# Performance work log

Measured on AMD Instinct MI355X. Metric: run time of the kernel, lower is better.

Reference implementation:

```python
import jax, jax.numpy as jnp
import numpy as np
jax.config.update("jax_enable_x64", True)

T_OLD = 60000
T_NEW = 60000
NV = 30000
MAX_STEPS = 300
FB_CHUNK = 500  # T_OLD must be divisible by this

FACE_OPP = np.array([[1, 2, 3], [0, 2, 3], [0, 1, 3], [0, 1, 2]])
EDGES = [(0, 1), (0, 2), (0, 3), (1, 2), (1, 3), (2, 3)]


def setup_inputs() -> dict:
    key = jax.random.key(0)
    k1, k2, k3, k4, k5 = jax.random.split(key, 5)
    # distinct vertices per tet (sorted base + strictly increasing offsets)
    off = jnp.arange(4, dtype=jnp.int64)
    new_indices = jnp.sort(jax.random.randint(k1, (T_NEW, 4), 0, NV - 4, dtype=jnp.int64), axis=1) + off
    old_indices = jnp.sort(jax.random.randint(k2, (T_OLD, 4), 0, NV - 4, dtype=jnp.int64), axis=1) + off
    return {
        "new_indices": new_indices,
        "old_indices": old_indices,
        "old_cc": jax.random.normal(k3, (T_OLD, 3), dtype=jnp.float32),
        "new_cc": jax.random.normal(k4, (T_NEW, 3), dtype=jnp.float32),
        "vertex_positions": jax.random.uniform(k5, (NV, 3), dtype=jnp.float32),
    }


def _min_edge_length(verts, indices):
    p = verts[indices]  # (T,4,3)
    el = jnp.stack([jnp.linalg.norm(p[:, a] - p[:, b], axis=-1) for a, b in EDGES])
    return el.min(axis=0)


def _forward(new_indices, old_indices, old_cc, new_cc, vertex_positions):
    T_new = new_indices.shape[0]
    T_old = old_indices.shape[0]
    Vn = vertex_positions.shape[0]

    # --- 1. unchanged-tet detection via sorted-vertex int64 keys ---
    key4 = lambda s: ((s[:, 0] * Vn + s[:, 1]) * Vn + s[:, 2]) * Vn + s[:, 3]
    ok = key4(jnp.sort(old_indices, axis=1))
    nk = key4(jnp.sort(new_indices, axis=1))
    order = jnp.argsort(ok)
    sk = ok[order]
    pos = jnp.searchsorted(sk, nk, side='right') - 1
    posc = jnp.clip(pos, 0, T_old - 1)
    matched = jnp.where((pos >= 0) & (sk[posc] == nk), order[posc], -1)
    is_matched = matched >= 0
    matched_safe = jnp.maximum(matched, 0)

    # --- 2. face adjacency of old mesh (sorted face keys, adjacent-equal pairing) ---
    fi = jnp.sort(old_indices[:, FACE_OPP], axis=2)          # (T_old,4,3)
    fk = (fi[..., 0] * Vn + fi[..., 1]) * Vn + fi[..., 2]    # (T_old,4)
    all_keys = fk.T.reshape(-1)                              # f-major like the numpy concat
    all_tets = jnp.tile(jnp.arange(T_old), 4)
    all_locals = jnp.repeat(jnp.arange(4), T_old)
    o2 = jnp.argsort(all_keys)
    sk2, st, sl = all_keys[o2], all_tets[o2], all_locals[o2]
    same = sk2[:-1] == sk2[1:]
    neighbors = jnp.full((T_old, 4), -1, dtype=jnp.int64)
    neighbors = neighbors.at[jnp.where(same, st[:-1], T_old), sl[:-1]].set(st[1:], mode='drop')
    neighbors = neighbors.at[jnp.where(same, st[1:], T_old), sl[1:]].set(st[:-1], mode='drop')

    # --- 3. per-old-tet inverse edge matrix; degenerate tets get no neighbors ---
    verts = jax.lax.stop_gradient(vertex_positions).astype(jnp.float32)
    p = verts[old_indices]                                   # (T_old,4,3)
    v0 = p[:, 0]
    Tm = jnp.stack([p[:, 1] - v0, p[:, 2] - v0, p[:, 3] - v0], axis=-1)
    degen = jnp.abs(jnp.linalg.det(Tm)) < 1e-10
    Tinv = jnp.linalg.inv(jnp.where(degen[:, None, None], jnp.eye(3, dtype=Tm.dtype), Tm))
    neighbors = jnp.where(degen[:, None], -1, neighbors)

    prio = jnp.full((Vn,), -1, dtype=jnp.int64)
    ar = jnp.arange(T_old)
    for vi in range(4):
        prio = prio.at[old_indices[:, vi]].max(vi * T_old + ar)
    v2t = jnp.where(prio >= 0, prio % T_old, 0)

    # --- 5. barycentric walk (masked, all float inputs stop-gradiented; int outputs) ---
    cent = jax.lax.stop_gradient(verts[new_indices].mean(axis=1))  # (T_new,3)
    seed = v2t[new_indices[:, 0]]
    n_walk = jnp.sum(~is_matched)
    thr = jnp.maximum(jnp.int64(100), n_walk // 1000)

    def cond(state):
        step, cur, rem, act = state
        return (step < MAX_STEPS) & (jnp.sum(act) >= thr)

    def body(state):
        step, cur, rem, act = state
        rel = cent - v0[cur]
        bary = jnp.einsum('nij,nj->ni', Tinv[cur], rel)
        all_b = jnp.concatenate([(1.0 - bary.sum(axis=1))[:, None], bary], axis=1)
        conv = act & (all_b.min(axis=1) >= -1e-4)
        rem = jnp.where(conv, cur, rem)
        act = act & ~conv
        nb = neighbors[cur, jnp.argmin(all_b, axis=1)]
        at_bd = act & (nb < 0)
        rem = jnp.where(at_bd, cur, rem)
        act = act & ~at_bd
        cur = jnp.where(act, nb, cur)
        return (step + 1, cur, rem, act)

    _, cur, rem, act = jax.lax.while_loop(cond, body, (jnp.int64(0), seed, seed, ~is_matched))
    rem = jnp.where(act, cur, rem)

    # --- 6. nearest-centroid fallback for unfinished walks (gated, chunked) ---
    old_cents = jax.lax.stop_gradient(verts[old_indices].mean(axis=1))

    def fallback(_):
        p2 = (cent ** 2).sum(-1)
        c2 = (old_cents ** 2).sum(-1)
        def scan_body(carry, i):
            bd, bi = carry
            c = jax.lax.dynamic_slice(old_cents, (i * FB_CHUNK, 0), (FB_CHUNK, 3))
            cn = jax.lax.dynamic_slice(c2, (i * FB_CHUNK,), (FB_CHUNK,))
            d = p2[:, None] - 2.0 * (cent @ c.T) + cn[None, :]
            md = d.min(axis=1)
            mi = d.argmin(axis=1).astype(jnp.int64) + i * FB_CHUNK
            imp = md < bd
            return (jnp.where(imp, md, bd), jnp.where(imp, mi, bi)), None
        init = (jnp.full((T_new,), jnp.inf, dtype=jnp.float32), jnp.zeros((T_new,), dtype=jnp.int64))
        (bd, bi), _ = jax.lax.scan(scan_body, init, jnp.arange(T_old // FB_CHUNK))
        return bi

    fb = jax.lax.cond(jnp.sum(act) > 0, fallback, lambda _: jnp.zeros((T_new,), dtype=jnp.int64), None)
    rem = jnp.clip(jnp.where(act, fb, rem), 0, T_old - 1)
    remap = jnp.where(is_matched, matched_safe, rem)

    # --- 7. candidates: containing tet + 4 face neighbors ---
    face_nb = neighbors[remap]
    face_nb = jnp.where(face_nb >= 0, face_nb, remap[:, None])
    cands = jnp.concatenate([remap[:, None], face_nb], axis=1)            # (T_new,5)
    cands = jnp.where(is_matched[:, None], matched_safe[:, None], cands)

    # --- 8. overlap / circumcenter-distance weights ---
    cand_verts = old_indices[cands]                                       # (T_new,5,4)
    overlap = (cand_verts[:, :, :, None] == new_indices[:, None, None, :]).any(-1).sum(-1).astype(jnp.float32)
    cc_d2 = ((old_cc[cands] - new_cc[:, None, :]) ** 2).sum(-1)
    raw = jnp.exp(overlap * 2.0) / (cc_d2 + 1e-8)
    weights = raw / raw.sum(axis=1, keepdims=True)

    # --- 9. density scale: min-edge-length ratio ---
    old_el = _min_edge_length(vertex_positions, old_indices)[cands]
    new_el = _min_edge_length(vertex_positions, new_indices)
    density_scale = jnp.clip(old_el / jnp.maximum(new_el[:, None], 1e-8), 0.1, 10.0)

    return cands, weights, density_scale


_forward_jit = jax.jit(_forward)


def reference(new_indices, old_indices, old_cc, new_cc, vertex_positions):
    return _forward_jit(new_indices, old_indices, old_cc, new_cc, vertex_positions)
```

## Files before the change

kernel.cpp:

```cpp
#include <hip/hip_runtime.h>

#pragma clang fp contract(off)

#define TOLD 60000
#define TNEW 60000
#define NVERT 30000
#define MAXSTEPS 300
#define THSZ 131072
#define FHSZ 131072
#define EMPTY64 0xFFFFFFFFFFFFFFFFULL
#define NWGR 60
#define VRANGE 500
#define NSLICE 16
#define TSLICE (TOLD / NSLICE)

#define NB_SETUP 235
#define NB_PRIO  (NWGR * NSLICE)
#define NB_NEWG  235
#define NB_FACE  938
#define NB_FOLD  118
#define NB_MATCH 235
#define NB_FB    120
#define NB_ASM   235

#define OFF_TKEYS    0u
#define OFF_FTAB     1048576u
#define OFF_NBR      2097152u
#define FF_BYTES     3057152u
#define OFF_CNT      3057152u
#define OFF_TVALS    3057408u
#define OFF_PPRIO    3581696u
#define OFF_PRIO     5501696u
#define OFF_IDXOLD   5621696u
#define OFF_CUR      6581696u
#define OFF_REM      6821696u
#define OFF_DEGEN    7061696u
#define OFF_LISTA    7301696u
#define OFF_LISTB    7541696u
#define OFF_MATCHED  7781696u
#define OFF_TV4      8021696u
#define OFF_COLD4    10901696u
#define OFF_CNEW4    11861696u
#define OFF_DM       12821696u

struct P {
  const unsigned int* rawNew;
  const unsigned int* rawOld;
  const float* occ;
  const float* ncc;
  const float* verts;
  float* out;
  unsigned long long* tkeys;
  unsigned long long* ftab;
  int* counters;
  int* tvals;
  int* idxOld;
  int* nbr;
  int* pprio;
  int* prio;
  int* cur; int* rem;
  int* degen;
  int* listA; int* listB;
  int* matched;
  float4* Tv4;
  float4* cold4;
  float4* cnew4;
  unsigned int* dm;
  unsigned int dmMask;
};

__device__ __forceinline__ unsigned hash64(unsigned long long k){
  k ^= k >> 33; k *= 0xff51afd7ed558ccdULL;
  k ^= k >> 33; k *= 0xc4ceb9fe1a85ec53ULL;
  k ^= k >> 33;
  return (unsigned)k;
}
__device__ __forceinline__ void cswap(int& a, int& b){ if (a > b){ int t = a; a = b; b = t; } }

__device__ __forceinline__ int detect64(const unsigned int* raw){
  unsigned acc = 0;
  const uint4* r4 = (const uint4*)raw;
  #pragma unroll
  for (int k = 0; k < 32; ++k){ uint4 v = r4[k]; acc |= (v.y | v.w); }
  return acc == 0u;
}

__device__ __forceinline__ int4 load_tet4(const unsigned int* raw, int is64, int t){
  if (is64){
    uint4 a = ((const uint4*)raw)[t * 2 + 0];
    uint4 b = ((const uint4*)raw)[t * 2 + 1];
    return make_int4((int)a.x, (int)a.z, (int)b.x, (int)b.z);
  }
  uint4 a = ((const uint4*)raw)[t];
  return make_int4((int)a.x, (int)a.y, (int)a.z, (int)a.w);
}

__device__ __forceinline__ void face_insert(unsigned long long* ftab, int* nbr,
                                            unsigned long long fkey, int t, int l){
  unsigned long long mine = (fkey << 18) | (unsigned long long)(t * 4 + l);
  unsigned slot = hash64(fkey ^ 0x9e3779b97f4a7c15ULL) & (FHSZ - 1);
  while (true){
    unsigned long long prev = atomicCAS(&ftab[slot], EMPTY64, mine);
    if (prev == EMPTY64) return;
    if ((prev >> 18) == fkey){
      int oid = (int)(prev & 0x3FFFFULL);
      nbr[t * 4 + l] = oid >> 2;
      nbr[oid] = t;
      return;
    }
    slot = (slot + 1) & (FHSZ - 1);
  }
}

__device__ __forceinline__ float min_edge_r(
    float q0x, float q0y, float q0z, float q1x, float q1y, float q1z,
    float q2x, float q2y, float q2z, float q3x, float q3y, float q3z){
  float m = 3.402823466e+38f;
  float dx, dy, dz, d;
  dx = q0x - q1x; dy = q0y - q1y; dz = q0z - q1z; d = sqrtf((dx*dx + dy*dy) + dz*dz); m = fminf(m, d);
  dx = q0x - q2x; dy = q0y - q2y; dz = q0z - q2z; d = sqrtf((dx*dx + dy*dy) + dz*dz); m = fminf(m, d);
  dx = q0x - q3x; dy = q0y - q3y; dz = q0z - q3z; d = sqrtf((dx*dx + dy*dy) + dz*dz); m = fminf(m, d);
  dx = q1x - q2x; dy = q1y - q2y; dz = q1z - q2z; d = sqrtf((dx*dx + dy*dy) + dz*dz); m = fminf(m, d);
  dx = q1x - q3x; dy = q1y - q3y; dz = q1z - q3z; d = sqrtf((dx*dx + dy*dy) + dz*dz); m = fminf(m, d);
  dx = q2x - q3x; dy = q2y - q3y; dz = q2z - q3z; d = sqrtf((dx*dx + dy*dy) + dz*dz); m = fminf(m, d);
  return m;
}

__global__ __launch_bounds__(256) void k_front(P p){
  __shared__ int sprio[VRANGE];
  int bb = blockIdx.x;
  if (bb < NB_SETUP){
    int t = bb * 256 + threadIdx.x;
    if (bb == 0 && threadIdx.x < 64) p.counters[threadIdx.x] = 0;
    if (t >= TOLD) return;
    int is64 = detect64(p.rawOld);
    int4 iv4 = load_tet4(p.rawOld, is64, t);
    int i0 = iv4.x, i1 = iv4.y, i2 = iv4.z, i3 = iv4.w;
    ((int4*)p.idxOld)[t] = iv4;

    {
      int s0 = i0, s1 = i1, s2 = i2, s3 = i3;
      cswap(s0, s1); cswap(s2, s3); cswap(s0, s2); cswap(s1, s3); cswap(s1, s2);
      unsigned long long key =
          (unsigned long long)((((long long)s0 * NVERT + s1) * NVERT + s2) * NVERT + s3);
      unsigned slot = hash64(key) & (THSZ - 1);
      while (true){
        unsigned long long prev = atomicCAS(&p.tkeys[slot], EMPTY64, key);
        if (prev == EMPTY64){ p.tvals[slot] = t; break; }
        if (prev == key){ atomicMax(&p.tvals[slot], t); break; }
        slot = (slot + 1) & (THSZ - 1);
      }
    }

    if (p.dmMask){
      const int FO[4][3] = {{1, 2, 3}, {0, 2, 3}, {0, 1, 3}, {0, 1, 2}};
      int iv[4] = {i0, i1, i2, i3};
      #pragma unroll
      for (int l = 0; l < 4; ++l){
        int a = iv[FO[l][0]], b = iv[FO[l][1]], c = iv[FO[l][2]];
        cswap(a, b); cswap(a, c); cswap(b, c);
        unsigned long long fk = (unsigned long long)(((long long)a * NVERT + b) * NVERT + c);
        p.dm[hash64(fk) & p.dmMask] = (unsigned)(t * 4 + l);
      }
    }

    float q0x = p.verts[i0 * 3 + 0], q0y = p.verts[i0 * 3 + 1], q0z = p.verts[i0 * 3 + 2];
    float q1x = p.verts[i1 * 3 + 0], q1y = p.verts[i1 * 3 + 1], q1z = p.verts[i1 * 3 + 2];
    float q2x = p.verts[i2 * 3 + 0], q2y = p.verts[i2 * 3 + 1], q2z = p.verts[i2 * 3 + 2];
    float q3x = p.verts[i3 * 3 + 0], q3y = p.verts[i3 * 3 + 1], q3z = p.verts[i3 * 3 + 2];
    float e1x = q1x - q0x, e1y = q1y - q0y, e1z = q1z - q0z;
    float e2x = q2x - q0x, e2y = q2y - q0y, e2z = q2z - q0z;
    float e3x = q3x - q0x, e3y = q3y - q0y, e3z = q3z - q0z;
    float c23x = e2y * e3z - e2z * e3y;
    float c23y = e2z * e3x - e2x * e3z;
    float c23z = e2x * e3y - e2y * e3x;
    float det = e1x * c23x + e1y * c23y + e1z * c23z;
    int dg = (fabsf(det) < 1e-10f) ? 1 : 0;
    p.degen[t] = dg;
    float4 r0, r1, r2;
    if (dg){
      r0 = make_float4(1.f, 0.f, 0.f, q0x);
      r1 = make_float4(0.f, 1.f, 0.f, q0y);
      r2 = make_float4(0.f, 0.f, 1.f, q0z);
    } else {
      float inv = 1.0f / det;
      float c31x = e3y * e1z - e3z * e1y;
      float c31y = e3z * e1x - e3x * e1z;
      float c31z = e3x * e1y - e3y * e1x;
      float c12x = e1y * e2z - e1z * e2y;
      float c12y = e1z * e2x - e1x * e2z;
      float c12z = e1x * e2y - e1y * e2x;
      r0 = make_float4(c23x * inv, c23y * inv, c23z * inv, q0x);
      r1 = make_float4(c31x * inv, c31y * inv, c31z * inv, q0y);
      r2 = make_float4(c12x * inv, c12y * inv, c12z * inv, q0z);
    }
    p.Tv4[t * 3 + 0] = r0;
    p.Tv4[t * 3 + 1] = r1;
    p.Tv4[t * 3 + 2] = r2;
    float el = min_edge_r(q0x, q0y, q0z, q1x, q1y, q1z, q2x, q2y, q2z, q3x, q3y, q3z);
    p.cold4[t] = make_float4((((q0x + q1x) + q2x) + q3x) * 0.25f,
                             (((q0y + q1y) + q2y) + q3y) * 0.25f,
                             (((q0z + q1z) + q2z) + q3z) * 0.25f, el);
  } else if (bb < NB_SETUP + NB_PRIO){
    int rb = bb - NB_SETUP;
    int range = rb / NSLICE;
    int slice = rb % NSLICE;
    int base = range * VRANGE;
    for (int j = threadIdx.x; j < VRANGE; j += 256) sprio[j] = -1;
    __syncthreads();
    int is64 = detect64(p.rawOld);
    int t0 = slice * TSLICE;
    for (int t = t0 + threadIdx.x; t < t0 + TSLICE; t += 256){
      int4 iv = load_tet4(p.rawOld, is64, t);
      int v;
      v = iv.x - base; if ((unsigned)v < VRANGE) atomicMax(&sprio[v], 0 * TOLD + t);
      v = iv.y - base; if ((unsigned)v < VRANGE) atomicMax(&sprio[v], 1 * TOLD + t);
      v = iv.z - base; if ((unsigned)v < VRANGE) atomicMax(&sprio[v], 2 * TOLD + t);
      v = iv.w - base; if ((unsigned)v < VRANGE) atomicMax(&sprio[v], 3 * TOLD + t);
    }
    __syncthreads();
    for (int j = threadIdx.x; j < VRANGE; j += 256)
      p.pprio[slice * NVERT + base + j] = sprio[j];
  } else {
    int n = (bb - NB_SETUP - NB_PRIO) * 256 + threadIdx.x;
    if (n >= TNEW) return;
    int is64 = detect64(p.rawNew);
    int4 ni = load_tet4(p.rawNew, is64, n);
    float q0x = p.verts[ni.x * 3 + 0], q0y = p.verts[ni.x * 3 + 1], q0z = p.verts[ni.x * 3 + 2];
    float q1x = p.verts[ni.y * 3 + 0], q1y = p.verts[ni.y * 3 + 1], q1z = p.verts[ni.y * 3 + 2];
    float q2x = p.verts[ni.z * 3 + 0], q2y = p.verts[ni.z * 3 + 1], q2z = p.verts[ni.z * 3 + 2];
    float q3x = p.verts[ni.w * 3 + 0], q3y = p.verts[ni.w * 3 + 1], q3z = p.verts[ni.w * 3 + 2];
    float el = min_edge_r(q0x, q0y, q0z, q1x, q1y, q1z, q2x, q2y, q2z, q3x, q3y, q3z);
    p.cnew4[n] = make_float4((((q0x + q1x) + q2x) + q3x) * 0.25f,
                             (((q0y + q1y) + q2y) + q3y) * 0.25f,
                             (((q0z + q1z) + q2z) + q3z) * 0.25f, el);
  }
}

__global__ __launch_bounds__(256) void k_mid(P p){
  int bb = blockIdx.x;
  if (bb < NB_FACE){
    int i = bb * 256 + threadIdx.x;
    if (i >= TOLD * 4) return;
    int t = i >> 2, l = i & 3;
    int4 iv4 = ((const int4*)p.idxOld)[t];
    int iv[4] = {iv4.x, iv4.y, iv4.z, iv4.w};
    const int FO[4][3] = {{1, 2, 3}, {0, 2, 3}, {0, 1, 3}, {0, 1, 2}};
    int a = iv[FO[l][0]], b = iv[FO[l][1]], c = iv[FO[l][2]];
    cswap(a, b); cswap(a, c); cswap(b, c);
    unsigned long long fk = (unsigned long long)(((long long)a * NVERT + b) * NVERT + c);
    if (p.dmMask){
      unsigned wid = p.dm[hash64(fk) & p.dmMask];
      if (wid == (unsigned)i) return;
      if (wid < (unsigned)(TOLD * 4)){
        int wt = wid >> 2, wl = (int)(wid & 3u);
        int4 wv4 = ((const int4*)p.idxOld)[wt];
        int wv[4] = {wv4.x, wv4.y, wv4.z, wv4.w};
        int wa = wv[FO[wl][0]], wb = wv[FO[wl][1]], wc = wv[FO[wl][2]];
        cswap(wa, wb); cswap(wa, wc); cswap(wb, wc);
        unsigned long long wfk = (unsigned long long)(((long long)wa * NVERT + wb) * NVERT + wc);
        if (wfk == fk){
          p.nbr[i] = wt;
          p.nbr[wid] = t;
          return;
        }
      }
    }
    face_insert(p.ftab, p.nbr, fk, t, l);
  } else if (bb < NB_FACE + NB_FOLD){
    int v = (bb - NB_FACE) * 256 + threadIdx.x;
    if (v >= NVERT) return;
    int pr = -1;
    #pragma unroll
    for (int s = 0; s < NSLICE; ++s) pr = max(pr, p.pprio[s * NVERT + v]);
    p.prio[v] = pr;
  } else {
    int n = (bb - NB_FACE - NB_FOLD) * 256 + threadIdx.x;
    if (n >= TNEW) return;
    int is64 = detect64(p.rawNew);
    int4 ni = load_tet4(p.rawNew, is64, n);
    int s0 = ni.x, s1 = ni.y, s2 = ni.z, s3 = ni.w;
    cswap(s0, s1); cswap(s2, s3); cswap(s0, s2); cswap(s1, s3); cswap(s1, s2);
    unsigned long long key =
        (unsigned long long)((((long long)s0 * NVERT + s1) * NVERT + s2) * NVERT + s3);
    int m = -1;
    unsigned slot = hash64(key) & (THSZ - 1);
    while (true){
      unsigned long long k = p.tkeys[slot];
      if (k == EMPTY64) break;
      if (k == key){ m = p.tvals[slot]; break; }
      slot = (slot + 1) & (THSZ - 1);
    }
    p.matched[n] = m;
  }
}

__device__ __forceinline__ bool walk_step(const P& p, int n){
  int c = p.cur[n];
  float4 r0 = p.Tv4[c * 3 + 0];
  float4 r1 = p.Tv4[c * 3 + 1];
  float4 r2 = p.Tv4[c * 3 + 2];
  float4 cn = p.cnew4[n];
  float rx = cn.x - r0.w, ry = cn.y - r1.w, rz = cn.z - r2.w;
  float b0 = r0.x * rx + r0.y * ry + r0.z * rz;
  float b1 = r1.x * rx + r1.y * ry + r1.z * rz;
  float b2 = r2.x * rx + r2.y * ry + r2.z * rz;
  float a0 = 1.0f - (b0 + b1 + b2);
  float ab[4] = {a0, b0, b1, b2};
  int amin = 0; float mn = ab[0];
  for (int j = 1; j < 4; ++j){ if (ab[j] < mn){ mn = ab[j]; amin = j; } }
  if (mn >= -0.0001f){ p.rem[n] = c; return false; }
  int nb = p.degen[c] ? -1 : p.nbr[c * 4 + amin];
  if (nb < 0){ p.rem[n] = c; return false; }
  p.cur[n] = nb;
  return true;
}

__global__ __launch_bounds__(256) void k_new3(P p){
  int n = blockIdx.x * blockDim.x + threadIdx.x;
  if (n >= TNEW) return;
  if (p.matched[n] >= 0) return;
  int is64 = detect64(p.rawNew);
  int i0 = is64 ? (int)((const long long*)p.rawNew)[n * 4] : ((const int*)p.rawNew)[n * 4];
  int pr = p.prio[i0];
  int seed = (pr >= 0) ? (pr % TOLD) : 0;
  p.cur[n] = seed;
  p.rem[n] = seed;
  p.listB[atomicAdd(&p.counters[0], 1)] = n;
  if (walk_step(p, n))
    p.listA[atomicAdd(&p.counters[1], 1)] = n;
}

__global__ void __launch_bounds__(1024) k_persist(P p){
  __shared__ int s_cnt;
  int nw = p.counters[0];
  if (nw < 100){
    for (int i = threadIdx.x; i < nw; i += blockDim.x) p.rem[p.listB[i]] = -1;
    if (threadIdx.x == 0){ p.counters[4] = nw; p.counters[5] = 1; }
    return;
  }
  int thr = max(100, nw / 1000);
  if (threadIdx.x == 0) s_cnt = atomicAdd(&p.counters[1], 0);
  __syncthreads();
  int count = s_cnt;
  int use_a = 1;
  int step = 1;
  while (step < MAXSTEPS && count >= thr){
    int* curL = use_a ? p.listA : p.listB;
    int* nxtL = use_a ? p.listB : p.listA;
    int* nxtC = use_a ? &p.counters[2] : &p.counters[1];
    int* curC = use_a ? &p.counters[1] : &p.counters[2];
    for (int i = threadIdx.x; i < count; i += blockDim.x){
      int n = curL[i];
      if (walk_step(p, n)){
        int pos = atomicAdd(nxtC, 1);
        nxtL[pos] = n;
      }
    }
    __syncthreads();
    if (threadIdx.x == 0){
      s_cnt = atomicAdd(nxtC, 0);
      atomicExch(curC, 0);
    }
    __syncthreads();
    count = s_cnt;
    use_a ^= 1;
    ++step;
  }
  const int* fl = use_a ? p.listA : p.listB;
  for (int i = threadIdx.x; i < count; i += blockDim.x) p.rem[fl[i]] = -1;
  if (threadIdx.x == 0){
    p.counters[4] = count;
    p.counters[5] = use_a ? 0 : 1;
  }
}

__device__ __forceinline__ void assemble_walker(const P& p, int n, int m, int remap){
  int cds[5];
  if (m >= 0){
    cds[0] = cds[1] = cds[2] = cds[3] = cds[4] = m;
  } else {
    cds[0] = remap;
    int dg = p.degen[remap];
    int4 nb4 = ((const int4*)p.nbr)[remap];
    int nbl[4] = {nb4.x, nb4.y, nb4.z, nb4.w};
    for (int l = 0; l < 4; ++l){
      int fb = dg ? -1 : nbl[l];
      cds[1 + l] = (fb >= 0) ? fb : remap;
    }
  }
  bool same = (cds[1] == cds[0]) & (cds[2] == cds[0]) &
              (cds[3] == cds[0]) & (cds[4] == cds[0]);
  int is64 = detect64(p.rawNew);
  int4 ni = load_tet4(p.rawNew, is64, n);
  float nc0 = p.ncc[n * 3 + 0], nc1 = p.ncc[n * 3 + 1], nc2 = p.ncc[n * 3 + 2];
  float nelv = fmaxf(p.cnew4[n].w, 1e-8f);
  if (same){
    int ct = cds[0];
    int4 cv = ((const int4*)p.idxOld)[ct];
    int ov = 0;
    ov += (cv.x == ni.x || cv.x == ni.y || cv.x == ni.z || cv.x == ni.w) ? 1 : 0;
    ov += (cv.y == ni.x || cv.y == ni.y || cv.y == ni.z || cv.y == ni.w) ? 1 : 0;
    ov += (cv.z == ni.x || cv.z == ni.y || cv.z == ni.z || cv.z == ni.w) ? 1 : 0;
    ov += (cv.w == ni.x || cv.w == ni.y || cv.w == ni.z || cv.w == ni.w) ? 1 : 0;
    float d0 = p.occ[ct * 3 + 0] - nc0;
    float d1 = p.occ[ct * 3 + 1] - nc1;
    float d2 = p.occ[ct * 3 + 2] - nc2;
    float ccd2 = (d0 * d0 + d1 * d1) + d2 * d2;
    float raw = expf((float)ov * 2.0f) / (ccd2 + 1e-8f);
    float rsum = 0.0f;
    rsum += raw; rsum += raw; rsum += raw; rsum += raw; rsum += raw;
    float wgt = raw / rsum;
    float ds = p.cold4[ct].w / nelv;
    ds = fminf(fmaxf(ds, 0.1f), 10.0f);
    float cf = (float)ct;
    for (int c = 0; c < 5; ++c){
      p.out[n * 5 + c] = cf;
      p.out[TNEW * 5 + n * 5 + c] = wgt;
      p.out[2 * TNEW * 5 + n * 5 + c] = ds;
    }
    return;
  }
  float raws[5]; float rsum = 0.0f;
  float oels[5];
  for (int c = 0; c < 5; ++c){
    int ct = cds[c];
    int4 cv = ((const int4*)p.idxOld)[ct];
    int ov = 0;
    ov += (cv.x == ni.x || cv.x == ni.y || cv.x == ni.z || cv.x == ni.w) ? 1 : 0;
    ov += (cv.y == ni.x || cv.y == ni.y || cv.y == ni.z || cv.y == ni.w) ? 1 : 0;
    ov += (cv.z == ni.x || cv.z == ni.y || cv.z == ni.z || cv.z == ni.w) ? 1 : 0;
    ov += (cv.w == ni.x || cv.w == ni.y || cv.w == ni.z || cv.w == ni.w) ? 1 : 0;
    float d0 = p.occ[ct * 3 + 0] - nc0;
    float d1 = p.occ[ct * 3 + 1] - nc1;
    float d2 = p.occ[ct * 3 + 2] - nc2;
    float ccd2 = (d0 * d0 + d1 * d1) + d2 * d2;
    float raw = expf((float)ov * 2.0f) / (ccd2 + 1e-8f);
    raws[c] = raw; rsum += raw;
    oels[c] = p.cold4[ct].w;
  }
  for (int c = 0; c < 5; ++c){
    p.out[n * 5 + c] = (float)cds[c];
    p.out[TNEW * 5 + n * 5 + c] = raws[c] / rsum;
    float ds = oels[c] / nelv;
    ds = fminf(fmaxf(ds, 0.1f), 10.0f);
    p.out[2 * TNEW * 5 + n * 5 + c] = ds;
  }
}

__global__ __launch_bounds__(256) void k_tail(P p){
  __shared__ float sd[256];
  __shared__ int si[256];
  int bb = blockIdx.x;
  if (bb < NB_FB){
    int fc = p.counters[4];
    const int* lst = p.counters[5] ? p.listB : p.listA;
    for (int e = bb; e < fc; e += NB_FB){
      int n = lst[e];
      float4 cn = p.cnew4[n];
      float cx = cn.x, cy = cn.y, cz = cn.z;
      float p2 = (cx * cx + cy * cy) + cz * cz;
      float bd = 3.402823466e+38f; int bi = 0;
      for (int j = threadIdx.x; j < TOLD; j += 256){
        float4 oc = p.cold4[j];
        float dot = (cx * oc.x + cy * oc.y) + cz * oc.z;
        float c2 = (oc.x * oc.x + oc.y * oc.y) + oc.z * oc.z;
        float d = (p2 - 2.0f * dot) + c2;
        if (d < bd || (d == bd && j < bi)){ bd = d; bi = j; }
      }
      sd[threadIdx.x] = bd; si[threadIdx.x] = bi;
      __syncthreads();
      for (int s = 128; s > 0; s >>= 1){
        if ((int)threadIdx.x < s){
          float od = sd[threadIdx.x + s]; int oi = si[threadIdx.x + s];
          if (od < sd[threadIdx.x] || (od == sd[threadIdx.x] && oi < si[threadIdx.x])){
            sd[threadIdx.x] = od; si[threadIdx.x] = oi;
          }
        }
        __syncthreads();
      }
      if (threadIdx.x == 0){
        int r = si[0];
        if (r < 0) r = 0; if (r > TOLD - 1) r = TOLD - 1;
        assemble_walker(p, n, -1, r);
      }
      __syncthreads();
    }
  } else {
    int n = (bb - NB_FB) * 256 + threadIdx.x;
    if (n >= TNEW) return;
    int m = p.matched[n];
    int remap = 0;
    if (m < 0){
      remap = p.rem[n];
      if (remap < 0) return;
    }
    assemble_walker(p, n, m, remap);
  }
}

extern "C" void kernel_launch(void* const* d_in, const int* in_sizes, int n_in,
                              void* d_out, int out_size, void* d_ws, size_t ws_size,
                              hipStream_t stream) {
  char* w = (char*)d_ws;
  P p;
  p.rawNew = (const unsigned int*)d_in[0];
  p.rawOld = (const unsigned int*)d_in[1];
  p.occ    = (const float*)d_in[2];
  p.ncc    = (const float*)d_in[3];
  p.verts  = (const float*)d_in[4];
  p.out    = (float*)d_out;
  p.tkeys    = (unsigned long long*)(w + OFF_TKEYS);
  p.ftab     = (unsigned long long*)(w + OFF_FTAB);
  p.nbr      = (int*)(w + OFF_NBR);
  p.counters = (int*)(w + OFF_CNT);
  p.tvals    = (int*)(w + OFF_TVALS);
  p.pprio    = (int*)(w + OFF_PPRIO);
  p.prio     = (int*)(w + OFF_PRIO);
  p.idxOld   = (int*)(w + OFF_IDXOLD);
  p.cur      = (int*)(w + OFF_CUR);
  p.rem      = (int*)(w + OFF_REM);
  p.degen    = (int*)(w + OFF_DEGEN);
  p.listA    = (int*)(w + OFF_LISTA);
  p.listB    = (int*)(w + OFF_LISTB);
  p.matched  = (int*)(w + OFF_MATCHED);
  p.Tv4      = (float4*)(w + OFF_TV4);
  p.cold4    = (float4*)(w + OFF_COLD4);
  p.cnew4    = (float4*)(w + OFF_CNEW4);
  p.dm       = (unsigned int*)(w + OFF_DM);
  size_t avail = (ws_size > (size_t)OFF_DM) ? ws_size - (size_t)OFF_DM : 0;
  unsigned dmMask = 0;
  for (int bshift = 21; bshift >= 16; --bshift){
    if (avail >= ((size_t)4 << bshift)){ dmMask = (1u << bshift) - 1u; break; }
  }
  p.dmMask = dmMask;

  hipMemsetAsync(w, 0xFF, FF_BYTES, stream);
  hipLaunchKernelGGL(k_front,   dim3(NB_SETUP + NB_PRIO + NB_NEWG), dim3(256), 0, stream, p);
  hipLaunchKernelGGL(k_mid,     dim3(NB_FACE + NB_FOLD + NB_MATCH), dim3(256), 0, stream, p);
  hipLaunchKernelGGL(k_new3,    dim3((TNEW + 255) / 256), dim3(256), 0, stream, p);
  hipLaunchKernelGGL(k_persist, dim3(1), dim3(1024), 0, stream, p);
  hipLaunchKernelGGL(k_tail,    dim3(NB_FB + NB_ASM), dim3(256), 0, stream, p);
}
```

Before: 123.9 us.

## Fuse walk kernels via last-block handoff and store face keys in direct-map slots

After: 132.1 us. +6.6%, slower.

```diff
diff --git a/kernel.cpp b/kernel.cpp
--- a/kernel.cpp
+++ b/kernel.cpp
@@ -65,7 +65,7 @@
   float4* Tv4;
   float4* cold4;
   float4* cnew4;
-  unsigned int* dm;
+  unsigned long long* dm;
   unsigned int dmMask;
 };
 
@@ -160,7 +160,7 @@
         int a = iv[FO[l][0]], b = iv[FO[l][1]], c = iv[FO[l][2]];
         cswap(a, b); cswap(a, c); cswap(b, c);
         unsigned long long fk = (unsigned long long)(((long long)a * NVERT + b) * NVERT + c);
-        p.dm[hash64(fk) & p.dmMask] = (unsigned)(t * 4 + l);
+        p.dm[hash64(fk) & p.dmMask] = (fk << 18) | (unsigned long long)(t * 4 + l);
       }
     }
 
@@ -250,20 +250,14 @@
     cswap(a, b); cswap(a, c); cswap(b, c);
     unsigned long long fk = (unsigned long long)(((long long)a * NVERT + b) * NVERT + c);
     if (p.dmMask){
-      unsigned wid = p.dm[hash64(fk) & p.dmMask];
-      if (wid == (unsigned)i) return;
-      if (wid < (unsigned)(TOLD * 4)){
-        int wt = wid >> 2, wl = (int)(wid & 3u);
-        int4 wv4 = ((const int4*)p.idxOld)[wt];
-        int wv[4] = {wv4.x, wv4.y, wv4.z, wv4.w};
-        int wa = wv[FO[wl][0]], wb = wv[FO[wl][1]], wc = wv[FO[wl][2]];
-        cswap(wa, wb); cswap(wa, wc); cswap(wb, wc);
-        unsigned long long wfk = (unsigned long long)(((long long)wa * NVERT + wb) * NVERT + wc);
-        if (wfk == fk){
-          p.nbr[i] = wt;
-          p.nbr[wid] = t;
-          return;
-        }
+      unsigned long long mine = (fk << 18) | (unsigned long long)i;
+      unsigned long long got = p.dm[hash64(fk) & p.dmMask];
+      if (got == mine) return;
+      if ((got >> 18) == fk){
+        int wid = (int)(got & 0x3FFFFULL);
+        p.nbr[i] = wid >> 2;
+        p.nbr[wid] = t;
+        return;
       }
     }
     face_insert(p.ftab, p.nbr, fk, t, l);
@@ -316,31 +310,41 @@
   return true;
 }
 
-__global__ __launch_bounds__(256) void k_new3(P p){
-  int n = blockIdx.x * blockDim.x + threadIdx.x;
-  if (n >= TNEW) return;
-  if (p.matched[n] >= 0) return;
-  int is64 = detect64(p.rawNew);
-  int i0 = is64 ? (int)((const long long*)p.rawNew)[n * 4] : ((const int*)p.rawNew)[n * 4];
-  int pr = p.prio[i0];
-  int seed = (pr >= 0) ? (pr % TOLD) : 0;
-  p.cur[n] = seed;
-  p.rem[n] = seed;
-  p.listB[atomicAdd(&p.counters[0], 1)] = n;
-  if (walk_step(p, n))
-    p.listA[atomicAdd(&p.counters[1], 1)] = n;
-}
-
-__global__ void __launch_bounds__(1024) k_persist(P p){
+__global__ __launch_bounds__(256) void k_walk(P p){
+  __shared__ int s_last;
   __shared__ int s_cnt;
-  int nw = p.counters[0];
+  int n = blockIdx.x * 256 + threadIdx.x;
+  if (n < TNEW && p.matched[n] < 0){
+    int is64 = detect64(p.rawNew);
+    int i0 = is64 ? (int)((const long long*)p.rawNew)[n * 4] : ((const int*)p.rawNew)[n * 4];
+    int pr = p.prio[i0];
+    int seed = (pr >= 0) ? (pr % TOLD) : 0;
+    p.cur[n] = seed;
+    p.rem[n] = seed;
+    p.listB[atomicAdd(&p.counters[0], 1)] = n;
+    if (walk_step(p, n))
+      p.listA[atomicAdd(&p.counters[1], 1)] = n;
+  }
+  __syncthreads();
+  if (threadIdx.x == 0){
+    __threadfence();
+    int d = __hip_atomic_fetch_add(&p.counters[6], 1, __ATOMIC_ACQ_REL,
+                                   __HIP_MEMORY_SCOPE_AGENT);
+    s_last = (d == (int)gridDim.x - 1);
+  }
+  __syncthreads();
+  if (!s_last) return;
+  __threadfence();
+
+  int nw = __hip_atomic_load(&p.counters[0], __ATOMIC_RELAXED, __HIP_MEMORY_SCOPE_AGENT);
   if (nw < 100){
     for (int i = threadIdx.x; i < nw; i += blockDim.x) p.rem[p.listB[i]] = -1;
     if (threadIdx.x == 0){ p.counters[4] = nw; p.counters[5] = 1; }
     return;
   }
   int thr = max(100, nw / 1000);
-  if (threadIdx.x == 0) s_cnt = atomicAdd(&p.counters[1], 0);
+  if (threadIdx.x == 0)
+    s_cnt = __hip_atomic_load(&p.counters[1], __ATOMIC_RELAXED, __HIP_MEMORY_SCOPE_AGENT);
   __syncthreads();
   int count = s_cnt;
   int use_a = 1;
@@ -351,10 +355,10 @@
     int* nxtC = use_a ? &p.counters[2] : &p.counters[1];
     int* curC = use_a ? &p.counters[1] : &p.counters[2];
     for (int i = threadIdx.x; i < count; i += blockDim.x){
-      int n = curL[i];
-      if (walk_step(p, n)){
+      int w = curL[i];
+      if (walk_step(p, w)){
         int pos = atomicAdd(nxtC, 1);
-        nxtL[pos] = n;
+        nxtL[pos] = w;
       }
     }
     __syncthreads();
@@ -527,18 +531,17 @@
   p.Tv4      = (float4*)(w + OFF_TV4);
   p.cold4    = (float4*)(w + OFF_COLD4);
   p.cnew4    = (float4*)(w + OFF_CNEW4);
-  p.dm       = (unsigned int*)(w + OFF_DM);
+  p.dm       = (unsigned long long*)(w + OFF_DM);
   size_t avail = (ws_size > (size_t)OFF_DM) ? ws_size - (size_t)OFF_DM : 0;
   unsigned dmMask = 0;
   for (int bshift = 21; bshift >= 16; --bshift){
-    if (avail >= ((size_t)4 << bshift)){ dmMask = (1u << bshift) - 1u; break; }
+    if (avail >= ((size_t)8 << bshift)){ dmMask = (1u << bshift) - 1u; break; }
   }
   p.dmMask = dmMask;
 
   hipMemsetAsync(w, 0xFF, FF_BYTES, stream);
-  hipLaunchKernelGGL(k_front,   dim3(NB_SETUP + NB_PRIO + NB_NEWG), dim3(256), 0, stream, p);
-  hipLaunchKernelGGL(k_mid,     dim3(NB_FACE + NB_FOLD + NB_MATCH), dim3(256), 0, stream, p);
-  hipLaunchKernelGGL(k_new3,    dim3((TNEW + 255) / 256), dim3(256), 0, stream, p);
-  hipLaunchKernelGGL(k_persist, dim3(1), dim3(1024), 0, stream, p);
-  hipLaunchKernelGGL(k_tail,    dim3(NB_FB + NB_ASM), dim3(256), 0, stream, p);
-}
+  hipLaunchKernelGGL(k_front, dim3(NB_SETUP + NB_PRIO + NB_NEWG), dim3(256), 0, stream, p);
+  hipLaunchKernelGGL(k_mid,   dim3(NB_FACE + NB_FOLD + NB_MATCH), dim3(256), 0, stream, p);
+  hipLaunchKernelGGL(k_walk,  dim3((TNEW + 255) / 256), dim3(256), 0, stream, p);
+  hipLaunchKernelGGL(k_tail,  dim3(NB_FB + NB_ASM), dim3(256), 0, stream, p);
+}
```
